# Kernel tuning notes

Measured on AMD Instinct MI355X. Metric: run time of the kernel, lower is better.

The kernel has to match this reference:

```python
import jax, jax.numpy as jnp
import numpy as np

B, S, D, H = 2, 2048, 1024, 16
DH = D // H  # 64


def setup_inputs() -> dict:
    key = jax.random.key(0)
    ks = jax.random.split(key, 10)
    inp = {
        "q": jax.random.normal(ks[0], (B, S, D), jnp.float32),
        "k": jax.random.normal(ks[1], (B, S, D), jnp.float32),
        "v": jax.random.normal(ks[2], (B, S, D), jnp.float32),
        "mask": jax.random.randint(ks[3], (B, S), 0, 2, jnp.int32),
        "Wq": jax.random.normal(ks[4], (D, D), jnp.float32) * 0.02,
        "bq": jnp.zeros((D,), jnp.float32),
        "Wk": jax.random.normal(ks[5], (D, D), jnp.float32) * 0.02,
        "bk": jnp.zeros((D,), jnp.float32),
        "Wv": jax.random.normal(ks[6], (D, D), jnp.float32) * 0.02,
        "bv": jnp.zeros((D,), jnp.float32),
    }
    return inp


def _split_heads(x):
    # [B, S, D] -> [B, H, S, DH]
    b, s, _ = x.shape
    return x.reshape(b, s, H, DH).transpose(0, 2, 1, 3)


def reference(q, k, v, mask, Wq, bq, Wk, bk, Wv, bv):
    qh = _split_heads(q @ Wq + bq)
    kh = _split_heads(k @ Wk + bk)
    vh = _split_heads(v @ Wv + bv)
    # NOTE: original scales by sqrt(hidden_size), not sqrt(head_dim)
    scores = jnp.einsum("bhqd,bhkd->bhqk", qh, kh) / jnp.sqrt(jnp.float32(D))
    m = mask.astype(jnp.float32)[:, None, None, :]  # [B,1,1,S_k]
    scores = scores + (-1e9) * (1.0 - m)
    weights = jax.nn.softmax(scores, axis=-1)
    out = jnp.einsum("bhqk,bhkd->bhqd", weights, vh)
    # concat heads: [B,H,S,DH] -> [B,S,D]
    return out.transpose(0, 2, 1, 3).reshape(q.shape[0], -1, D)
```

## Files before the change

### kernel.cpp

```cpp
#include <hip/hip_runtime.h>


#define B_ 2
#define S_ 2048
#define D_ 1024
#define H_ 16
#define DH_ 64
#define M_ (B_*S_)

#define WT_OFF  ((size_t)3*4194304)
#define XB_OFF  (WT_OFF + (size_t)3*1048576)

typedef __attribute__((ext_vector_type(8))) short short8;
typedef __attribute__((ext_vector_type(4))) float f32x4;
typedef __attribute__((ext_vector_type(4))) unsigned int u32x4;
#define MFMA16(a,b,c) __builtin_amdgcn_mfma_f32_16x16x32_bf16(a,b,c,0,0,0)

typedef __attribute__((address_space(1))) const void* gptr_t;
typedef __attribute__((address_space(3))) void* lptr_t;
static __device__ inline void gload_lds16(const void* g, void* l) {
    __builtin_amdgcn_global_load_lds((gptr_t)g, (lptr_t)l, 16, 0, 0);
}

static __device__ inline unsigned short f2bf(float x) {
    union { float f; unsigned u; } v; v.f = x;
    return (unsigned short)((v.u + 0x7fffu + ((v.u >> 16) & 1u)) >> 16);
}
static __device__ inline unsigned packp(float a, float b) {
    return __builtin_amdgcn_perm(__float_as_uint(b) + 0x8000u,
                                 __float_as_uint(a) + 0x8000u, 0x07060302u);
}
static __device__ inline unsigned cvtpk(float a, float b) {
    unsigned r;
    asm("v_cvt_pk_bf16_f32 %0, %1, %2" : "=v"(r) : "v"(a), "v"(b));
    return r;
}

__global__ __launch_bounds__(256) void convert_all(
    const float* __restrict__ X0, const float* __restrict__ X1,
    const float* __restrict__ X2,
    const float* __restrict__ Wq, const float* __restrict__ Wk,
    const float* __restrict__ Wv,
    unsigned short* __restrict__ O0, unsigned short* __restrict__ O1,
    unsigned short* __restrict__ O2, unsigned short* __restrict__ WtBase)
{
    __shared__ unsigned short T[64][72];
    const int z = blockIdx.z;
    const int t = threadIdx.x;

    if (blockIdx.x < 4096) {
        const float* X = z==0 ? X0 : (z==1 ? X1 : X2);
        unsigned short* O = z==0 ? O0 : (z==1 ? O1 : O2);
        int idx = blockIdx.x*256 + t;
        float4 xv = *(const float4*)&X[(size_t)idx*4];
        uint2 o;
        o.x = (unsigned)f2bf(xv.x) | ((unsigned)f2bf(xv.y) << 16);
        o.y = (unsigned)f2bf(xv.z) | ((unsigned)f2bf(xv.w) << 16);
        *(uint2*)&O[(size_t)idx*4] = o;
        return;
    }

    const float* W = z==0 ? Wq : (z==1 ? Wk : Wv);
    unsigned short* Out = WtBase + ((size_t)z << 20);
    const int bx2 = blockIdx.x - 4096;
    const int n0 = (bx2 & 15)*64, k0 = (bx2 >> 4)*64;
    const int tk = t >> 4, tn4 = (t & 15)*4;

    #pragma unroll
    for (int i=0;i<4;i++){
        int kk = tk + i*16;
        float4 wv = *(const float4*)&W[(size_t)(k0+kk)*D_ + n0 + tn4];
        T[tn4+0][kk] = f2bf(wv.x);
        T[tn4+1][kk] = f2bf(wv.y);
        T[tn4+2][kk] = f2bf(wv.z);
        T[tn4+3][kk] = f2bf(wv.w);
    }
    __syncthreads();

    const int n = t >> 2, seg = t & 3;
    uint4 a = *(uint4*)&T[n][seg*16];
    uint4 b = *(uint4*)&T[n][seg*16 + 8];
    *(uint4*)&Out[(size_t)(n0+n)*D_ + k0 + seg*16]     = a;
    *(uint4*)&Out[(size_t)(n0+n)*D_ + k0 + seg*16 + 8] = b;
}

__global__ __launch_bounds__(256) void proj_gemm(
    const unsigned short* __restrict__ A0, const unsigned short* __restrict__ A1,
    const unsigned short* __restrict__ A2, const unsigned short* __restrict__ WtBase,
    const float* __restrict__ b0, const float* __restrict__ b1,
    const float* __restrict__ b2, unsigned short* __restrict__ OutBase)
{
    const int lin0 = blockIdx.x + (blockIdx.y << 3) + (blockIdx.z << 8);
    const int swz  = (lin0 & 7)*96 + (lin0 >> 3);
    const int bxn  = swz & 7;
    const int byn  = (swz >> 3) & 31;
    const int which = swz >> 8;

    const unsigned short* A  = which==0 ? A0 : (which==1 ? A1 : A2);
    const unsigned short* Bm = WtBase + ((size_t)which << 20);
    const float* bias        = which==0 ? b0 : (which==1 ? b1 : b2);
    unsigned short* Out      = OutBase + ((size_t)which << 22);
    const float oscale = (which==0) ? 0.04508422f : 1.0f;

    __shared__ __align__(16) unsigned short As[128*64];
    __shared__ __align__(16) unsigned short Bs[128*64];

    const int t    = threadIdx.x;
    const int m0   = byn * 128;
    const int n0   = bxn * 128;
    const int w    = t >> 6;
    const int lane = t & 63;
    const int l15  = lane & 15;
    const int quad = lane >> 4;
    const int wm   = w >> 1, wn = w & 1;

    f32x4 acc[4][4];
    #pragma unroll
    for (int i=0;i<4;i++)
        #pragma unroll
        for (int j=0;j<4;j++) acc[i][j] = (f32x4){0.f,0.f,0.f,0.f};

    float biasv[4];
    #pragma unroll
    for (int nt=0; nt<4; nt++)
        biasv[nt] = bias[n0 + wn*64 + nt*16 + l15];

    int sArow[4], sAkc[4];
    #pragma unroll
    for (int i=0;i<4;i++){
        int s  = (w*4 + i)*64 + lane;
        int r  = s >> 3, cs = s & 7;
        sArow[i] = r;
        sAkc[i]  = ((cs ^ (r & 7)) * 8);
    }

    for (int ks = 0; ks < 16; ++ks) {
        const int kb = ks * 64;
        #pragma unroll
        for (int i=0;i<4;i++){
            int s = (w*4 + i)*64 + lane;
            gload_lds16(A  + (size_t)(m0 + sArow[i])*D_ + kb + sAkc[i], (unsigned short*)As + s*8);
            gload_lds16(Bm + (size_t)(n0 + sArow[i])*D_ + kb + sAkc[i], (unsigned short*)Bs + s*8);
        }
        __syncthreads();

        #pragma unroll
        for (int kh=0; kh<2; kh++){
            short8 aF[4], bF[4];
            #pragma unroll
            for (int mt=0; mt<4; mt++){
                int r  = wm*64 + mt*16 + l15;
                int cs = (kh*4 + quad) ^ (r & 7);
                aF[mt] = *(const short8*)(As + r*64 + cs*8);
            }
            #pragma unroll
            for (int nt=0; nt<4; nt++){
                int r  = wn*64 + nt*16 + l15;
                int cs = (kh*4 + quad) ^ (r & 7);
                bF[nt] = *(const short8*)(Bs + r*64 + cs*8);
            }
            #pragma unroll
            for (int mt=0; mt<4; mt++)
                #pragma unroll
                for (int nt=0; nt<4; nt++)
                    acc[mt][nt] = MFMA16(aF[mt], bF[nt], acc[mt][nt]);
        }
        __syncthreads();
    }

    if (which != 2) {
        #pragma unroll
        for (int nt=0; nt<4; nt++){
            int n  = n0 + wn*64 + nt*16 + l15;
            int hh = n >> 6, dh = n & 63;
            #pragma unroll
            for (int mt=0; mt<4; mt++){
                #pragma unroll
                for (int r=0; r<4; r++){
                    int m  = m0 + wm*64 + mt*16 + quad*4 + r;
                    int bb = m >> 11, ss = m & (S_-1);
                    float v = (acc[mt][nt][r] + biasv[nt]) * oscale;
                    Out[((size_t)((bb*H_ + hh)*S_ + ss))*DH_ + dh] = f2bf(v);
                }
            }
        }
    } else {
        #pragma unroll
        for (int nt=0; nt<4; nt++){
            int n  = n0 + wn*64 + nt*16 + l15;
            int hh = n >> 6, dh = n & 63;
            #pragma unroll
            for (int mt=0; mt<4; mt++){
                int m  = m0 + wm*64 + mt*16 + quad*4;
                int bb = m >> 11, ss = m & (S_-1);
                uint2 pk;
                pk.x = packp(acc[mt][nt][0] + biasv[nt], acc[mt][nt][1] + biasv[nt]);
                pk.y = packp(acc[mt][nt][2] + biasv[nt], acc[mt][nt][3] + biasv[nt]);
                *(uint2*)&Out[((size_t)((bb*H_ + hh)*DH_ + dh))*S_ + ss] = pk;
            }
        }
    }
}

__global__ __launch_bounds__(512, 2) void attn_kernel(
    const unsigned short* __restrict__ ws, const int* __restrict__ mask,
    float* __restrict__ out)
{
    const unsigned short* Qh = ws;
    const unsigned short* Kh = ws + (size_t)M_*D_;
    const unsigned short* Vg = ws + 2*(size_t)M_*D_;

    const int lin = blockIdx.x + (blockIdx.y << 3) + (blockIdx.z << 7);
    const int Wn  = (lin & 7)*32 + (lin >> 3);
    const int qt = Wn & 7;
    const int h  = (Wn >> 3) & 15;
    const int bb = Wn >> 7;

    const size_t base = ((size_t)(bb*H_ + h)) * S_ * DH_;
    const int q0 = qt * 256;

    __shared__ __align__(16) unsigned char smem[73728];
    unsigned short* KsB = (unsigned short*)smem;
    unsigned short* VtB = (unsigned short*)(smem + 32768);
    float*          MsT = (float*)(smem + 65536);
    float*          Ob  = (float*)smem;

    const int t    = threadIdx.x;
    const int w    = t >> 6;
    const int lane = t & 63;
    const int l15  = lane & 15;
    const int quad = lane >> 4;

    short8 qf[2][2];
    #pragma unroll
    for (int qs=0; qs<2; qs++){
        const unsigned short* qp = Qh + base + (size_t)(q0 + w*32 + qs*16 + l15)*DH_ + quad*8;
        qf[qs][0] = *(const short8*)(qp);
        qf[qs][1] = *(const short8*)(qp + 32);
    }

    f32x4 accO[2][4];
    #pragma unroll
    for (int qs=0; qs<2; qs++)
        #pragma unroll
        for (int i=0;i<4;i++) accO[qs][i] = (f32x4){0.f,0.f,0.f,0.f};
    f32x4 lv[2] = {(f32x4){0.f,0.f,0.f,0.f}, (f32x4){0.f,0.f,0.f,0.f}};

    int rr[2], cc[2], ssl[2], gK[2];
    #pragma unroll
    for (int i=0;i<2;i++){
        int s  = (w*2 + i)*64 + lane;
        int r  = s >> 3, cs = s & 7;
        int r6 = r & 63;
        ssl[i] = s;
        rr[i]  = r;
        cc[i]  = (cs ^ (r & 7)) * 8;
        gK[i]  = (r & 64) + ((r6 >> 4) & 1)*32 + ((r6 >> 2) & 3)*8 + (r6 >> 5)*4 + (r6 & 3);
    }

    #define ISSUE128(k0v, p) do {                                              \
        _Pragma("unroll")                                                      \
        for (int i=0;i<2;i++){                                                 \
            gload_lds16(Kh + base + (size_t)((k0v) + gK[i])*DH_ + cc[i],       \
                        KsB + (p)*8192 + ssl[i]*8);                            \
            gload_lds16(Vg + base + (size_t)(rr[i] & 63)*S_ + (k0v)            \
                            + (rr[i] & 64) + cc[i],                            \
                        VtB + (p)*8192 + ssl[i]*8);                            \
        }                                                                      \
    } while(0)

    ISSUE128(0, 0);
    #pragma unroll
    for (int i=0;i<4;i++){
        int idx = i*512 + t;
        MsT[idx] = mask[bb*S_ + idx] ? 0.f : -1e9f;
    }
    __syncthreads();

    for (int it = 0; it < 16; ++it){
        const int p = it & 1;
        if (it < 15) ISSUE128((it+1)*128, 1-p);

        #pragma unroll
        for (int sbi = 0; sbi < 2; ++sbi){
            const int sb = sbi ^ (w & 1);
            const unsigned short* Ks  = KsB + p*8192 + sb*4096;
            const unsigned short* Vts = VtB + p*8192 + sb*4096;
            const float*          Mp  = MsT + it*128 + sb*64;

            f32x4 msv[4];
            #pragma unroll
            for (int st=0; st<4; st++)
                msv[st] = *(const f32x4*)&Mp[(st&1)*32 + (st>>1)*4 + quad*8];

            short8 ka[4], kb[4];
            #pragma unroll
            for (int st=0; st<4; st++){
                int row = st*16 + l15;
                const unsigned short* kr = Ks + row*64;
                ka[st] = *(const short8*)(kr + ((quad    ) ^ (row & 7))*8);
                kb[st] = *(const short8*)(kr + ((quad + 4) ^ (row & 7))*8);
            }
            short8 vf[4][2];
            #pragma unroll
            for (int mt=0; mt<4; mt++){
                int row = mt*16 + l15;
                const unsigned short* vr = Vts + row*64;
                vf[mt][0] = *(const short8*)(vr + ((quad    ) ^ (row & 7))*8);
                vf[mt][1] = *(const short8*)(vr + ((quad + 4) ^ (row & 7))*8);
            }

            #pragma unroll
            for (int qs=0; qs<2; qs++){
                f32x4 sc[4];
                __builtin_amdgcn_s_setprio(1);
                #pragma unroll
                for (int st=0; st<4; st++){
                    f32x4 a = msv[st];
                    a = MFMA16(ka[st], qf[qs][0], a);
                    a = MFMA16(kb[st], qf[qs][1], a);
                    sc[st] = a;
                }
                __builtin_amdgcn_s_setprio(0);
                f32x4 pvv[4];
                #pragma unroll
                for (int st=0; st<4; st++)
                    #pragma unroll
                    for (int rj=0; rj<4; rj++)
                        pvv[st][rj] = __builtin_amdgcn_exp2f(sc[st][rj]);
                f32x4 s01 = pvv[0] + pvv[1];
                f32x4 s23 = pvv[2] + pvv[3];
                lv[qs] += (s01 + s23);
                u32x4 u0 = { cvtpk(pvv[0][0],pvv[0][1]), cvtpk(pvv[0][2],pvv[0][3]),
                             cvtpk(pvv[2][0],pvv[2][1]), cvtpk(pvv[2][2],pvv[2][3]) };
                u32x4 u1 = { cvtpk(pvv[1][0],pvv[1][1]), cvtpk(pvv[1][2],pvv[1][3]),
                             cvtpk(pvv[3][0],pvv[3][1]), cvtpk(pvv[3][2],pvv[3][3]) };
                short8 pf0 = __builtin_bit_cast(short8, u0);
                short8 pf1 = __builtin_bit_cast(short8, u1);
                __builtin_amdgcn_s_setprio(1);
                #pragma unroll
                for (int mt=0; mt<4; mt++){
                    accO[qs][mt] = MFMA16(vf[mt][0], pf0, accO[qs][mt]);
                    accO[qs][mt] = MFMA16(vf[mt][1], pf1, accO[qs][mt]);
                }
                __builtin_amdgcn_s_setprio(0);
            }
        }
        __syncthreads();
    }

    #pragma unroll
    for (int qs=0; qs<2; qs++){
        float l = (lv[qs][0] + lv[qs][1]) + (lv[qs][2] + lv[qs][3]);
        l += __shfl_xor(l, 16);
        l += __shfl_xor(l, 32);
        float invl = 1.0f / fmaxf(l, 1e-30f);
        #pragma unroll
        for (int mt=0; mt<4; mt++)
            #pragma unroll
            for (int r=0; r<4; r++)
                Ob[(w*32 + qs*16 + l15)*68 + mt*16 + quad*4 + r] = accO[qs][mt][r]*invl;
    }
    __syncthreads();

    #pragma unroll
    for (int i=0;i<8;i++){
        int f  = (i*512 + t)*4;
        int qq = f >> 6, dh = f & 63;
        float4 o = *(float4*)&Ob[qq*68 + dh];
        *(float4*)&out[((size_t)(bb*S_ + q0 + qq))*D_ + h*DH_ + dh] = o;
    }
    #undef ISSUE128
}

extern "C" void kernel_launch(void* const* d_in, const int* in_sizes, int n_in,
                              void* d_out, int out_size, void* d_ws, size_t ws_size,
                              hipStream_t stream) {
    const float* q    = (const float*)d_in[0];
    const float* k    = (const float*)d_in[1];
    const float* v    = (const float*)d_in[2];
    const int*   mask = (const int*)d_in[3];
    const float* Wq   = (const float*)d_in[4];
    const float* b0   = (const float*)d_in[5];
    const float* Wk   = (const float*)d_in[6];
    const float* b1   = (const float*)d_in[7];
    const float* Wv   = (const float*)d_in[8];
    const float* b2   = (const float*)d_in[9];
    float* out = (float*)d_out;
    unsigned short* ws = (unsigned short*)d_ws;

    unsigned short* xq = ws + XB_OFF;
    unsigned short* xk = (unsigned short*)d_out;
    unsigned short* xv = (unsigned short*)d_out + 4194304;

    convert_all<<<dim3(4352,1,3), 256, 0, stream>>>(q, k, v, Wq, Wk, Wv,
                                                    xq, xk, xv, ws + WT_OFF);
    proj_gemm<<<dim3(8,32,3), 256, 0, stream>>>(xq, xk, xv, ws + WT_OFF,
                                                b0, b1, b2, ws);
    attn_kernel<<<dim3(8,16,2), 512, 0, stream>>>(ws, mask, out);
}
```

Measured before the change: 196.6 us.

## Double-buffer projection GEMM LDS loads and widen input conversion per thread

The projection GEMM now uses two LDS buffers and issues the global-to-LDS loads for the next K step before computing on the current one. It waits with an explicit vmcnt and raw barriers instead of __syncthreads, so memory latency can overlap the MFMA work. Separately, the fp32-to-bf16 input conversion handles 8 elements per thread with 16-byte stores, which halves the block count. The GEMM now needs twice the LDS, which may reduce occupancy, and correctness depends on the vmcnt accounting being exact.

```diff
diff --git a/kernel.cpp b/kernel.cpp
--- a/kernel.cpp
+++ b/kernel.cpp
@@ -48,21 +48,24 @@
     const int z = blockIdx.z;
     const int t = threadIdx.x;
 
-    if (blockIdx.x < 4096) {
+    if (blockIdx.x < 2048) {
         const float* X = z==0 ? X0 : (z==1 ? X1 : X2);
         unsigned short* O = z==0 ? O0 : (z==1 ? O1 : O2);
-        int idx = blockIdx.x*256 + t;
-        float4 xv = *(const float4*)&X[(size_t)idx*4];
-        uint2 o;
-        o.x = (unsigned)f2bf(xv.x) | ((unsigned)f2bf(xv.y) << 16);
-        o.y = (unsigned)f2bf(xv.z) | ((unsigned)f2bf(xv.w) << 16);
-        *(uint2*)&O[(size_t)idx*4] = o;
+        size_t e = ((size_t)(blockIdx.x*256 + t))*8;
+        float4 a = *(const float4*)&X[e];
+        float4 b = *(const float4*)&X[e+4];
+        uint4 o;
+        o.x = (unsigned)f2bf(a.x) | ((unsigned)f2bf(a.y) << 16);
+        o.y = (unsigned)f2bf(a.z) | ((unsigned)f2bf(a.w) << 16);
+        o.z = (unsigned)f2bf(b.x) | ((unsigned)f2bf(b.y) << 16);
+        o.w = (unsigned)f2bf(b.z) | ((unsigned)f2bf(b.w) << 16);
+        *(uint4*)&O[e] = o;
         return;
     }
 
     const float* W = z==0 ? Wq : (z==1 ? Wk : Wv);
     unsigned short* Out = WtBase + ((size_t)z << 20);
-    const int bx2 = blockIdx.x - 4096;
+    const int bx2 = blockIdx.x - 2048;
     const int n0 = (bx2 & 15)*64, k0 = (bx2 >> 4)*64;
     const int tk = t >> 4, tn4 = (t & 15)*4;
 
@@ -102,8 +105,8 @@
     unsigned short* Out      = OutBase + ((size_t)which << 22);
     const float oscale = (which==0) ? 0.04508422f : 1.0f;
 
-    __shared__ __align__(16) unsigned short As[128*64];
-    __shared__ __align__(16) unsigned short Bs[128*64];
+    __shared__ __align__(16) unsigned short As[2*128*64];
+    __shared__ __align__(16) unsigned short Bs[2*128*64];
 
     const int t    = threadIdx.x;
     const int m0   = byn * 128;
@@ -134,16 +137,32 @@
         sAkc[i]  = ((cs ^ (r & 7)) * 8);
     }
 
+    #define PISSUE(ksv, buf) do {                                              \
+        const int kb = (ksv)*64;                                               \
+        _Pragma("unroll")                                                      \
+        for (int i=0;i<4;i++){                                                 \
+            int s = (w*4 + i)*64 + lane;                                       \
+            gload_lds16(A  + (size_t)(m0 + sArow[i])*D_ + kb + sAkc[i],        \
+                        (unsigned short*)As + (buf)*8192 + s*8);               \
+            gload_lds16(Bm + (size_t)(n0 + sArow[i])*D_ + kb + sAkc[i],        \
+                        (unsigned short*)Bs + (buf)*8192 + s*8);               \
+        }                                                                      \
+    } while(0)
+
+    PISSUE(0, 0);
+    int cur = 0;
     for (int ks = 0; ks < 16; ++ks) {
-        const int kb = ks * 64;
-        #pragma unroll
-        for (int i=0;i<4;i++){
-            int s = (w*4 + i)*64 + lane;
-            gload_lds16(A  + (size_t)(m0 + sArow[i])*D_ + kb + sAkc[i], (unsigned short*)As + s*8);
-            gload_lds16(Bm + (size_t)(n0 + sArow[i])*D_ + kb + sAkc[i], (unsigned short*)Bs + s*8);
+        if (ks < 15) {
+            PISSUE(ks+1, cur^1);
+            asm volatile("s_waitcnt vmcnt(8)" ::: "memory");
+        } else {
+            asm volatile("s_waitcnt vmcnt(0)" ::: "memory");
         }
-        __syncthreads();
-
+        __builtin_amdgcn_s_barrier();
+        __builtin_amdgcn_sched_barrier(0);
+
+        const unsigned short* Asb = As + cur*8192;
+        const unsigned short* Bsb = Bs + cur*8192;
         #pragma unroll
         for (int kh=0; kh<2; kh++){
             short8 aF[4], bF[4];
@@ -151,13 +170,13 @@
             for (int mt=0; mt<4; mt++){
                 int r  = wm*64 + mt*16 + l15;
                 int cs = (kh*4 + quad) ^ (r & 7);
-                aF[mt] = *(const short8*)(As + r*64 + cs*8);
+                aF[mt] = *(const short8*)(Asb + r*64 + cs*8);
             }
             #pragma unroll
             for (int nt=0; nt<4; nt++){
                 int r  = wn*64 + nt*16 + l15;
                 int cs = (kh*4 + quad) ^ (r & 7);
-                bF[nt] = *(const short8*)(Bs + r*64 + cs*8);
+                bF[nt] = *(const short8*)(Bsb + r*64 + cs*8);
             }
             #pragma unroll
             for (int mt=0; mt<4; mt++)
@@ -165,7 +184,8 @@
                 for (int nt=0; nt<4; nt++)
                     acc[mt][nt] = MFMA16(aF[mt], bF[nt], acc[mt][nt]);
         }
-        __syncthreads();
+        __builtin_amdgcn_s_barrier();
+        cur ^= 1;
     }
 
     if (which != 2) {
@@ -200,6 +220,7 @@
             }
         }
     }
+    #undef PISSUE
 }
 
 __global__ __launch_bounds__(512, 2) void attn_kernel(
@@ -393,7 +414,7 @@
     unsigned short* xk = (unsigned short*)d_out;
     unsigned short* xv = (unsigned short*)d_out + 4194304;
 
-    convert_all<<<dim3(4352,1,3), 256, 0, stream>>>(q, k, v, Wq, Wk, Wv,
+    convert_all<<<dim3(2304,1,3), 256, 0, stream>>>(q, k, v, Wq, Wk, Wv,
                                                     xq, xk, xv, ws + WT_OFF);
     proj_gemm<<<dim3(8,32,3), 256, 0, stream>>>(xq, xk, xv, ws + WT_OFF,
                                                 b0, b1, b2, ws);
```

Result: faster. 190.3 us (-3.2%).
